# Optimization experiments

Measured on AMD Instinct MI355X. Metric: run time of the kernel, lower is better.

## Reference

```python
import jax, jax.numpy as jnp
import numpy as np
import math

D_MODEL = 1024
N_HEADS = 16
SPARSITY = 0.3


def setup_inputs() -> dict:
    key = jax.random.key(0)
    ks = jax.random.split(key, 12)
    B, S, D = 4, 2048, D_MODEL
    Dh = D // 2
    sc = 0.02
    inp = {
        "x": jax.random.normal(ks[0], (B, S, D), dtype=jnp.float32),
        "wq": jax.random.normal(ks[1], (D, D), dtype=jnp.float32) * sc,
        "bq": jnp.zeros((D,), jnp.float32),
        "wk": jax.random.normal(ks[2], (D, D), dtype=jnp.float32) * sc,
        "bk": jnp.zeros((D,), jnp.float32),
        "wv": jax.random.normal(ks[3], (D, D), dtype=jnp.float32) * sc,
        "bv": jnp.zeros((D,), jnp.float32),
        "wo": jax.random.normal(ks[4], (D, D), dtype=jnp.float32) * sc,
        "bo": jnp.zeros((D,), jnp.float32),
        "wi1": jax.random.normal(ks[5], (Dh, D), dtype=jnp.float32) * sc,
        "bi1": jnp.zeros((Dh,), jnp.float32),
        "wi2": jax.random.normal(ks[6], (1, Dh), dtype=jnp.float32) * sc,
        "bi2": jnp.zeros((1,), jnp.float32),
    }
    return inp


def reference(x, wq, bq, wk, bk, wv, bv, wo, bo, wi1, bi1, wi2, bi2):
    B, S, D = x.shape
    H = N_HEADS
    hd = D // H
    k = max(1, int(S * SPARSITY))

    # projections (torch Linear: x @ W^T + b)
    Q = (x @ wq.T + bq).reshape(B, S, H, hd).transpose(0, 2, 1, 3)  # [B,H,S,hd]
    K = (x @ wk.T + bk).reshape(B, S, H, hd).transpose(0, 2, 1, 3)
    V = (x @ wv.T + bv).reshape(B, S, H, hd).transpose(0, 2, 1, 3)

    # learned indexer -> per-position importance [B,S]
    h = jnp.maximum(x @ wi1.T + bi1, 0.0)
    importance = (h @ wi2.T + bi2)[..., 0]

    _, top_idx = jax.lax.top_k(importance, k)  # [B,k]
    sparse_mask = jnp.zeros((B, S), dtype=x.dtype).at[
        jnp.arange(B)[:, None], top_idx
    ].set(1.0)

    scores = jnp.einsum("bhqd,bhkd->bhqk", Q, K) / math.sqrt(hd)
    scores = jnp.where(sparse_mask[:, None, None, :] == 0, -jnp.inf, scores)
    attn = jax.nn.softmax(scores, axis=-1)

    out = jnp.einsum("bhqk,bhkd->bhqd", attn, V)
    out = out.transpose(0, 2, 1, 3).reshape(B, S, D)
    return out @ wo.T + bo
```

## Files before the change

### kernel.cpp

```cpp
#include <hip/hip_runtime.h>
#include <math.h>

#define BB 4
#define SS 2048
#define DD 1024
#define HHD 16
#define HD 64
#define DH 512
#define KSEL 614
#define KPAD 640
#define MTOT (BB*SS)
#define NCH (KPAD/64)
#define MKV (BB*KPAD)

typedef __attribute__((ext_vector_type(8))) short bf16x8;
typedef __attribute__((ext_vector_type(4))) float f32x4;

#define LDS_CAST(p) ((__attribute__((address_space(3))) void*)(p))
#define GLB_CAST(p) ((const __attribute__((address_space(1))) void*)(p))

#define QK_SCALE 0.18033688011112042f

__device__ inline short bf16rne(float v)
{
    unsigned u = __builtin_bit_cast(unsigned, v);
    return (short)((u + 0x7FFFu + ((u >> 16) & 1u)) >> 16);
}

__device__ inline void split1(float v, short& h, short& l)
{
    unsigned u = __builtin_bit_cast(unsigned, v);
    unsigned hr = (u + 0x7FFFu + ((u >> 16) & 1u)) >> 16;
    h = (short)hr;
    float hf = __builtin_bit_cast(float, hr << 16);
    float res = v - hf;
    unsigned u2 = __builtin_bit_cast(unsigned, res);
    unsigned lr = (u2 + 0x7FFFu + ((u2 >> 16) & 1u)) >> 16;
    l = (short)lr;
}

__global__ __launch_bounds__(256)
void split_convert(const float* __restrict__ in, short* __restrict__ hi,
                   short* __restrict__ lo, int n4)
{
    const int i = blockIdx.x * 256 + threadIdx.x;
    if (i >= n4) return;
    float4 v = reinterpret_cast<const float4*>(in)[i];
    short4 h, l;
    split1(v.x, h.x, l.x);
    split1(v.y, h.y, l.y);
    split1(v.z, h.z, l.z);
    split1(v.w, h.w, l.w);
    reinterpret_cast<short4*>(hi)[i] = h;
    reinterpret_cast<short4*>(lo)[i] = l;
}

__global__ __launch_bounds__(256)
void split_weights(const float* __restrict__ wq, const float* __restrict__ wk,
                   const float* __restrict__ wv, const float* __restrict__ wo,
                   const float* __restrict__ wi1,
                   short* __restrict__ Bqkv_hi, short* __restrict__ wo_hi,
                   short* __restrict__ Wi_hi, short* __restrict__ Wi_lo)
{
    const int i = blockIdx.x * 256 + threadIdx.x;
    const int which = blockIdx.y;
    if (which < 4) {
        const float* src = (which == 0) ? wq : (which == 1) ? wk : (which == 2) ? wv : wo;
        short* dst = (which == 3) ? wo_hi : (Bqkv_hi + (size_t)which * DD * DD);
        float4 v = reinterpret_cast<const float4*>(src)[i];
        short4 hh;
        hh.x = bf16rne(v.x); hh.y = bf16rne(v.y); hh.z = bf16rne(v.z); hh.w = bf16rne(v.w);
        reinterpret_cast<short4*>(dst)[i] = hh;
    } else {
        if (i >= DH*DD/4) return;
        float4 v = reinterpret_cast<const float4*>(wi1)[i];
        short4 h, l;
        split1(v.x, h.x, l.x); split1(v.y, h.y, l.y);
        split1(v.z, h.z, l.z); split1(v.w, h.w, l.w);
        reinterpret_cast<short4*>(Wi_hi)[i] = h;
        reinterpret_cast<short4*>(Wi_lo)[i] = l;
    }
}

__global__ __launch_bounds__(256)
void concat_bias2(const float* __restrict__ a, const float* __restrict__ b,
                  float* __restrict__ o)
{
    const int i = blockIdx.x * 256 + threadIdx.x;
    o[i] = (i < 1024) ? a[i] : b[i - 1024];
}

template<bool BF16_OUT, bool QSCALE>
__global__ __launch_bounds__(256)
void gemm_bf16(const short* __restrict__ Ahi, const short* __restrict__ Bhi,
               const float* __restrict__ bias, void* __restrict__ Cv,
               int M, int N, int K, int ldc)
{
    __shared__ short sAh[128*64];
    __shared__ short sBh[128*64];

    const int t = threadIdx.x;
    const int lane = t & 63, wid = t >> 6;
    const int wm = wid >> 1, wn = wid & 1;
    const int row0 = blockIdx.y * 128, col0 = blockIdx.x * 128;
    const int g = lane >> 4, r = lane & 15;
    const int lrow = lane >> 3;
    const int lslot = lane & 7;

    f32x4 acc[4][4];
    #pragma unroll
    for (int mt = 0; mt < 4; ++mt)
        #pragma unroll
        for (int nt = 0; nt < 4; ++nt) acc[mt][nt] = (f32x4){0.f, 0.f, 0.f, 0.f};

    for (int k0 = 0; k0 < K; k0 += 64) {
        #pragma unroll
        for (int e = 0; e < 4; ++e) {
            const int rl = wid * 32 + e * 8 + lrow;
            const int scol = k0 + ((lslot ^ (rl & 7)) << 3);
            const size_t ga = (size_t)(row0 + rl) * K + scol;
            const size_t gb = (size_t)(col0 + rl) * K + scol;
            const int ldso = (wid * 32 + e * 8) * 64;
            __builtin_amdgcn_global_load_lds(GLB_CAST(Ahi + ga), LDS_CAST(sAh + ldso), 16, 0, 0);
            __builtin_amdgcn_global_load_lds(GLB_CAST(Bhi + gb), LDS_CAST(sBh + ldso), 16, 0, 0);
        }
        __syncthreads();

        #pragma unroll
        for (int kk = 0; kk < 2; ++kk) {
            bf16x8 ah[4], bh[4];
            #pragma unroll
            for (int mt = 0; mt < 4; ++mt) {
                const int rw = wm * 64 + mt * 16 + r;
                ah[mt] = *reinterpret_cast<const bf16x8*>(sAh + rw * 64 + (((kk*4 + g) ^ (rw & 7)) << 3));
            }
            #pragma unroll
            for (int nt = 0; nt < 4; ++nt) {
                const int rw = wn * 64 + nt * 16 + r;
                bh[nt] = *reinterpret_cast<const bf16x8*>(sBh + rw * 64 + (((kk*4 + g) ^ (rw & 7)) << 3));
            }
            #pragma unroll
            for (int mt = 0; mt < 4; ++mt)
                #pragma unroll
                for (int nt = 0; nt < 4; ++nt)
                    acc[mt][nt] = __builtin_amdgcn_mfma_f32_16x16x32_bf16(ah[mt], bh[nt], acc[mt][nt], 0, 0, 0);
        }
        __syncthreads();
    }

    #pragma unroll
    for (int nt = 0; nt < 4; ++nt) {
        const int col = wn * 64 + nt * 16 + r;
        const float bv = bias[col0 + col];
        const bool qs = QSCALE && (col0 + col) < 1024;
        #pragma unroll
        for (int mt = 0; mt < 4; ++mt) {
            #pragma unroll
            for (int e = 0; e < 4; ++e) {
                const int row = row0 + wm * 64 + mt * 16 + 4 * g + e;
                float v = acc[mt][nt][e] + bv;
                if (qs) v *= QK_SCALE;
                if (BF16_OUT)
                    ((short*)Cv)[(size_t)row * ldc + col0 + col] = bf16rne(v);
                else
                    ((float*)Cv)[(size_t)row * ldc + col0 + col] = v;
            }
        }
    }
}

__global__ __launch_bounds__(256)
void gemm_kv_gather(const short* __restrict__ Ahi, const short* __restrict__ Bhi,
                    const int* __restrict__ idxg, const float* __restrict__ bias,
                    short* __restrict__ C)
{
    __shared__ short sAh[128*64];
    __shared__ short sBh[128*64];

    const int K = DD, N = 2048;
    const int t = threadIdx.x;
    const int lane = t & 63, wid = t >> 6;
    const int wm = wid >> 1, wn = wid & 1;
    const int row0 = blockIdx.y * 128, col0 = blockIdx.x * 128;
    const int g = lane >> 4, r = lane & 15;
    const int lrow = lane >> 3;
    const int lslot = lane & 7;

    size_t garow[4];
    #pragma unroll
    for (int e = 0; e < 4; ++e) {
        const int rl = row0 + wid * 32 + e * 8 + lrow;
        const int grow = (rl / KPAD) * SS + idxg[rl];
        garow[e] = (size_t)grow * K;
    }

    f32x4 acc[4][4];
    #pragma unroll
    for (int mt = 0; mt < 4; ++mt)
        #pragma unroll
        for (int nt = 0; nt < 4; ++nt) acc[mt][nt] = (f32x4){0.f, 0.f, 0.f, 0.f};

    for (int k0 = 0; k0 < K; k0 += 64) {
        #pragma unroll
        for (int e = 0; e < 4; ++e) {
            const int rl = wid * 32 + e * 8 + lrow;
            const int scol = k0 + ((lslot ^ (rl & 7)) << 3);
            const size_t gb = (size_t)(col0 + rl) * K + scol;
            const int ldso = (wid * 32 + e * 8) * 64;
            __builtin_amdgcn_global_load_lds(GLB_CAST(Ahi + garow[e] + scol), LDS_CAST(sAh + ldso), 16, 0, 0);
            __builtin_amdgcn_global_load_lds(GLB_CAST(Bhi + gb), LDS_CAST(sBh + ldso), 16, 0, 0);
        }
        __syncthreads();

        #pragma unroll
        for (int kk = 0; kk < 2; ++kk) {
            bf16x8 ah[4], bh[4];
            #pragma unroll
            for (int mt = 0; mt < 4; ++mt) {
                const int rw = wm * 64 + mt * 16 + r;
                ah[mt] = *reinterpret_cast<const bf16x8*>(sAh + rw * 64 + (((kk*4 + g) ^ (rw & 7)) << 3));
            }
            #pragma unroll
            for (int nt = 0; nt < 4; ++nt) {
                const int rw = wn * 64 + nt * 16 + r;
                bh[nt] = *reinterpret_cast<const bf16x8*>(sBh + rw * 64 + (((kk*4 + g) ^ (rw & 7)) << 3));
            }
            #pragma unroll
            for (int mt = 0; mt < 4; ++mt)
                #pragma unroll
                for (int nt = 0; nt < 4; ++nt)
                    acc[mt][nt] = __builtin_amdgcn_mfma_f32_16x16x32_bf16(ah[mt], bh[nt], acc[mt][nt], 0, 0, 0);
        }
        __syncthreads();
    }

    #pragma unroll
    for (int nt = 0; nt < 4; ++nt) {
        const int col = wn * 64 + nt * 16 + r;
        const float bv = bias[col0 + col];
        #pragma unroll
        for (int mt = 0; mt < 4; ++mt) {
            #pragma unroll
            for (int e = 0; e < 4; ++e) {
                const int row = row0 + wm * 64 + mt * 16 + 4 * g + e;
                C[(size_t)row * N + col0 + col] = bf16rne(acc[mt][nt][e] + bv);
            }
        }
    }
}

template<bool RELU>
__global__ __launch_bounds__(256)
void gemm_split64(const short* __restrict__ Ahi, const short* __restrict__ Alo,
                  const short* __restrict__ Bhi, const short* __restrict__ Blo,
                  const float* __restrict__ bias, float* __restrict__ C,
                  int M, int N, int K, int ldc)
{
    __shared__ short sAh[64*32];
    __shared__ short sAl[64*32];
    __shared__ short sBh[128*32];
    __shared__ short sBl[128*32];

    const int t = threadIdx.x;
    const int lane = t & 63, wid = t >> 6;
    const int row0 = blockIdx.y * 64, col0 = blockIdx.x * 128;
    const int g = lane >> 4, r = lane & 15;
    const int srow = lane >> 2;
    const int sslot = lane & 3;

    f32x4 acc[4][2];
    #pragma unroll
    for (int mt = 0; mt < 4; ++mt)
        #pragma unroll
        for (int nt = 0; nt < 2; ++nt) acc[mt][nt] = (f32x4){0.f, 0.f, 0.f, 0.f};

    for (int k0 = 0; k0 < K; k0 += 32) {
        {
            const int rl = wid * 16 + srow;
            const int scol = k0 + ((sslot ^ ((rl >> 2) & 3)) << 3);
            const size_t ga = (size_t)(row0 + rl) * K + scol;
            const int ldso = (wid * 16) * 32;
            __builtin_amdgcn_global_load_lds(GLB_CAST(Ahi + ga), LDS_CAST(sAh + ldso), 16, 0, 0);
            __builtin_amdgcn_global_load_lds(GLB_CAST(Alo + ga), LDS_CAST(sAl + ldso), 16, 0, 0);
        }
        #pragma unroll
        for (int i = 0; i < 2; ++i) {
            const int rl = i * 64 + wid * 16 + srow;
            const int scol = k0 + ((sslot ^ ((rl >> 2) & 3)) << 3);
            const size_t gb = (size_t)(col0 + rl) * K + scol;
            const int ldso = (i * 64 + wid * 16) * 32;
            __builtin_amdgcn_global_load_lds(GLB_CAST(Bhi + gb), LDS_CAST(sBh + ldso), 16, 0, 0);
            __builtin_amdgcn_global_load_lds(GLB_CAST(Blo + gb), LDS_CAST(sBl + ldso), 16, 0, 0);
        }
        __syncthreads();

        bf16x8 ah[4], al[4], bh[2], bl[2];
        #pragma unroll
        for (int mt = 0; mt < 4; ++mt) {
            const int row = mt * 16 + r;
            const int sw = g ^ ((row >> 2) & 3);
            ah[mt] = *reinterpret_cast<const bf16x8*>(sAh + row * 32 + sw * 8);
            al[mt] = *reinterpret_cast<const bf16x8*>(sAl + row * 32 + sw * 8);
        }
        #pragma unroll
        for (int nt = 0; nt < 2; ++nt) {
            const int row = wid * 32 + nt * 16 + r;
            const int sw = g ^ ((row >> 2) & 3);
            bh[nt] = *reinterpret_cast<const bf16x8*>(sBh + row * 32 + sw * 8);
            bl[nt] = *reinterpret_cast<const bf16x8*>(sBl + row * 32 + sw * 8);
        }
        #pragma unroll
        for (int mt = 0; mt < 4; ++mt)
            #pragma unroll
            for (int nt = 0; nt < 2; ++nt) {
                acc[mt][nt] = __builtin_amdgcn_mfma_f32_16x16x32_bf16(ah[mt], bh[nt], acc[mt][nt], 0, 0, 0);
                acc[mt][nt] = __builtin_amdgcn_mfma_f32_16x16x32_bf16(ah[mt], bl[nt], acc[mt][nt], 0, 0, 0);
                acc[mt][nt] = __builtin_amdgcn_mfma_f32_16x16x32_bf16(al[mt], bh[nt], acc[mt][nt], 0, 0, 0);
            }
        __syncthreads();
    }

    #pragma unroll
    for (int nt = 0; nt < 2; ++nt) {
        const int col = wid * 32 + nt * 16 + r;
        const float bv = bias[col0 + col];
        #pragma unroll
        for (int mt = 0; mt < 4; ++mt) {
            #pragma unroll
            for (int e = 0; e < 4; ++e) {
                const int row = row0 + mt * 16 + 4 * g + e;
                float v = acc[mt][nt][e] + bv;
                if (RELU) v = fmaxf(v, 0.f);
                C[(size_t)row * ldc + col0 + col] = v;
            }
        }
    }
}

__global__ __launch_bounds__(256)
void importance_kernel(const float* __restrict__ h, const float* __restrict__ wi2,
                       const float* __restrict__ bi2, float* __restrict__ imp)
{
    const int wid = threadIdx.x >> 6, lane = threadIdx.x & 63;
    const int row = blockIdx.x * 4 + wid;
    const float* hr = h + (size_t)row * DH;
    float s = 0.f;
    #pragma unroll
    for (int i = 0; i < DH/64; ++i)
        s = fmaf(hr[lane + i*64], wi2[lane + i*64], s);
    #pragma unroll
    for (int off = 32; off; off >>= 1) s += __shfl_down(s, off);
    if (lane == 0) imp[row] = s + bi2[0];
}

__global__ __launch_bounds__(256)
void rank_kernel(const float* __restrict__ imp, int* __restrict__ flags)
{
    __shared__ float simp[SS];
    const int b = blockIdx.y;
    const int t = threadIdx.x;
    const float* bimp = imp + b * SS;
    for (int i = t; i < SS/4; i += 256)
        reinterpret_cast<float4*>(simp)[i] = reinterpret_cast<const float4*>(bimp)[i];
    __syncthreads();

    const int i = blockIdx.x * 32 + (t >> 3);
    const int part = t & 7;
    const float v = simp[i];
    const float4* slice = reinterpret_cast<const float4*>(simp + part * (SS/8));
    const int jb = part * (SS/8);
    int rank = 0;
    #pragma unroll 8
    for (int jj = 0; jj < SS/32; ++jj) {
        const float4 u4 = slice[jj];
        const int j = jb + jj * 4;
        rank += (u4.x > v) || ((u4.x == v) && (j + 0 < i));
        rank += (u4.y > v) || ((u4.y == v) && (j + 1 < i));
        rank += (u4.z > v) || ((u4.z == v) && (j + 2 < i));
        rank += (u4.w > v) || ((u4.w == v) && (j + 3 < i));
    }
    rank += __shfl_xor(rank, 1);
    rank += __shfl_xor(rank, 2);
    rank += __shfl_xor(rank, 4);
    if (part == 0) flags[b * SS + i] = (rank < KSEL) ? 1 : 0;
}

__global__ __launch_bounds__(256)
void compact_kernel(const int* __restrict__ flags, int* __restrict__ idxg)
{
    __shared__ int sscan[SS];
    __shared__ int sidx[KSEL];
    const int b = blockIdx.x, t = threadIdx.x;
    for (int i = t; i < SS; i += 256) sscan[i] = flags[b * SS + i];
    __syncthreads();
    for (int off = 1; off < SS; off <<= 1) {
        int vals[SS/256];
        #pragma unroll
        for (int c = 0; c < SS/256; ++c) {
            const int i = t + c * 256;
            int v = sscan[i];
            if (i >= off) v += sscan[i - off];
            vals[c] = v;
        }
        __syncthreads();
        #pragma unroll
        for (int c = 0; c < SS/256; ++c) sscan[t + c * 256] = vals[c];
        __syncthreads();
    }
    for (int i = t; i < SS; i += 256) {
        const int f = flags[b * SS + i];
        if (f) sidx[sscan[i] - 1] = i;
    }
    __syncthreads();
    for (int p = t; p < KPAD; p += 256)
        idxg[b * KPAD + p] = sidx[min(p, KSEL - 1)];
}

__global__ __launch_bounds__(256)
void gather_kv(const short* __restrict__ KVc, short* __restrict__ Kg,
               short* __restrict__ Vg)
{
    __shared__ short Vs[64*72];
    const int t = threadIdx.x;
    const int c = blockIdx.x, h = blockIdx.y, b = blockIdx.z;
    const int srow = t >> 2;
    const int sq4  = t & 3;

    const size_t cbase = ((size_t)(b * HHD + h) * NCH + c) * 4096;

    const short* kb = KVc + (size_t)(b * KPAD + c * 64 + srow) * 2048 + h * HD + sq4 * 16;
    bf16x8 k0 = *reinterpret_cast<const bf16x8*>(kb);
    bf16x8 k1 = *reinterpret_cast<const bf16x8*>(kb + 8);
    short* kout = Kg + cbase + srow * HD + sq4 * 16;
    *reinterpret_cast<bf16x8*>(kout)     = k0;
    *reinterpret_cast<bf16x8*>(kout + 8) = k1;

    const short* vbp = kb + 1024;
    bf16x8 v0 = *reinterpret_cast<const bf16x8*>(vbp);
    bf16x8 v1 = *reinterpret_cast<const bf16x8*>(vbp + 8);
    #pragma unroll
    for (int j = 0; j < 8; ++j) {
        Vs[(sq4 * 16 + j) * 72 + srow]     = v0[j];
        Vs[(sq4 * 16 + 8 + j) * 72 + srow] = v1[j];
    }
    __syncthreads();

    const int x = 8 * (srow >> 4);
    short* vout = Vg + cbase + srow * 64;
    *reinterpret_cast<bf16x8*>(vout + ((sq4 * 16)     ^ x)) = *reinterpret_cast<const bf16x8*>(&Vs[srow * 72 + sq4 * 16]);
    *reinterpret_cast<bf16x8*>(vout + ((sq4 * 16 + 8) ^ x)) = *reinterpret_cast<const bf16x8*>(&Vs[srow * 72 + sq4 * 16 + 8]);
}

__global__ __launch_bounds__(512)
void attn_mfma(const short* __restrict__ Qb, const short* __restrict__ Kg,
               const short* __restrict__ Vg, short* __restrict__ AOhi)
{
    __shared__ short Ks[2][64*72];
    __shared__ short Vs[2][64*72];
    __shared__ short Ps[8][16*72];

    const int t = threadIdx.x;
    const int lane = t & 63, w = t >> 6;
    const int g = lane >> 4, r = lane & 15;
    const int qt = blockIdx.x, h = blockIdx.y, b = blockIdx.z;
    const int q0 = qt * 128;
    short* Psw = &Ps[w][0];

    const int srow = t >> 3;
    const int scol = (t & 7) * 8;
    const short* kcbase = Kg + ((size_t)(b * HHD + h) * NCH) * 4096 + srow * 64 + scol;
    const short* vcbase = Vg + ((size_t)(b * HHD + h) * NCH) * 4096 + srow * 64 + scol;

    bf16x8 qh[2];
    {
        const short* qrow = Qb + (size_t)(b * SS + q0 + w * 16 + r) * DD + h * HD;
        qh[0] = *reinterpret_cast<const bf16x8*>(qrow + 8 * g);
        qh[1] = *reinterpret_cast<const bf16x8*>(qrow + 32 + 8 * g);
    }

    bf16x8 ones;
    #pragma unroll
    for (int j = 0; j < 8; ++j) ones[j] = (short)0x3F80;

    f32x4 oacc[4];
    #pragma unroll
    for (int dt = 0; dt < 4; ++dt) oacc[dt] = (f32x4){0.f, 0.f, 0.f, 0.f};
    f32x4 dacc = (f32x4){0.f, 0.f, 0.f, 0.f};

    bf16x8 kreg = *reinterpret_cast<const bf16x8*>(kcbase);
    bf16x8 vreg = *reinterpret_cast<const bf16x8*>(vcbase);

    for (int c = 0; c < NCH; ++c) {
        const int cur = c & 1;
        *reinterpret_cast<bf16x8*>(&Ks[cur][srow*72 + scol]) = kreg;
        *reinterpret_cast<bf16x8*>(&Vs[cur][srow*72 + scol]) = vreg;
        if (c + 1 < NCH) {
            kreg = *reinterpret_cast<const bf16x8*>(kcbase + (size_t)(c + 1) * 4096);
            vreg = *reinterpret_cast<const bf16x8*>(vcbase + (size_t)(c + 1) * 4096);
        }
        __syncthreads();

        f32x4 sa[4];
        #pragma unroll
        for (int kt = 0; kt < 4; ++kt) {
            bf16x8 kf0 = *reinterpret_cast<const bf16x8*>(&Ks[cur][(kt*16 + r)*72 + 8*g]);
            bf16x8 kf1 = *reinterpret_cast<const bf16x8*>(&Ks[cur][(kt*16 + r)*72 + 32 + 8*g]);
            f32x4 s = (f32x4){0.f, 0.f, 0.f, 0.f};
            s = __builtin_amdgcn_mfma_f32_16x16x32_bf16(qh[0], kf0, s, 0, 0, 0);
            s = __builtin_amdgcn_mfma_f32_16x16x32_bf16(qh[1], kf1, s, 0, 0, 0);
            sa[kt] = s;
        }
        if (c == NCH - 1) {
            #pragma unroll
            for (int kt = 0; kt < 4; ++kt)
                if (c*64 + kt*16 + r >= KSEL)
                    sa[kt] = (f32x4){-INFINITY, -INFINITY, -INFINITY, -INFINITY};
        }

        #pragma unroll
        for (int kt = 0; kt < 4; ++kt)
            #pragma unroll
            for (int e = 0; e < 4; ++e)
                Psw[(4*g + e)*72 + ((kt*16 + r) ^ (8*g))] =
                    (short)(__builtin_bit_cast(unsigned, exp2f(sa[kt][e])) >> 16);

        #pragma unroll
        for (int kc = 0; kc < 2; ++kc) {
            bf16x8 pf = *reinterpret_cast<const bf16x8*>(&Psw[r*72 + kc*32 + 8*(g ^ (r >> 2))]);
            dacc = __builtin_amdgcn_mfma_f32_16x16x32_bf16(pf, ones, dacc, 0, 0, 0);
            #pragma unroll
            for (int dt = 0; dt < 4; ++dt) {
                bf16x8 vf = *reinterpret_cast<const bf16x8*>(&Vs[cur][(dt*16 + r)*72 + kc*32 + 8*(g ^ dt)]);
                oacc[dt] = __builtin_amdgcn_mfma_f32_16x16x32_bf16(pf, vf, oacc[dt], 0, 0, 0);
            }
        }
    }

    #pragma unroll
    for (int dt = 0; dt < 4; ++dt)
        #pragma unroll
        for (int e = 0; e < 4; ++e) {
            const size_t a = (size_t)(b * SS + q0 + w*16 + 4*g + e) * DD + h * HD + dt*16 + r;
            AOhi[a] = bf16rne(oacc[dt][e] / dacc[e]);
        }
}

extern "C" void kernel_launch(void* const* d_in, const int* in_sizes, int n_in,
                              void* d_out, int out_size, void* d_ws, size_t ws_size,
                              hipStream_t stream)
{
    const float* x   = (const float*)d_in[0];
    const float* wq  = (const float*)d_in[1];
    const float* bq  = (const float*)d_in[2];
    const float* wk  = (const float*)d_in[3];
    const float* bk  = (const float*)d_in[4];
    const float* wv  = (const float*)d_in[5];
    const float* bv  = (const float*)d_in[6];
    const float* wo  = (const float*)d_in[7];
    const float* bo  = (const float*)d_in[8];
    const float* wi1 = (const float*)d_in[9];
    const float* bi1 = (const float*)d_in[10];
    const float* wi2 = (const float*)d_in[11];
    const float* bi2 = (const float*)d_in[12];
    float* out = (float*)d_out;

    const size_t MB = 1ull << 20;
    char* W = (char*)d_ws;
    short* x_hi  = (short*)(W + 0);
    short* x_lo  = (short*)(W + 16*MB);
    short* Qb    = (short*)(W + 32*MB);
    short* KVc   = (short*)(W + 48*MB);
    short* Wi_hi = (short*)(W + 96*MB);
    short* Wi_lo = (short*)(W + 97*MB);
    short* Bqkv_hi=(short*)(W + 128*MB);
    short* wo_hi = (short*)(W + 134*MB);
    float* Hw    = (float*)(W + 144*MB);
    short* Kg    = (short*)(W + 144*MB);
    short* Vg    = (short*)(W + 150*MB);
    float* bkv   = (float*)(W + 160*MB);
    float* imp   = (float*)(W + 160*MB + 64*1024);
    int*   flags = (int*)(W + 160*MB + 128*1024);
    int*   idxg  = (int*)(W + 160*MB + 192*1024);
    short* AO_hi = x_hi;

    const size_t NM = (size_t)MTOT * DD;

    split_convert<<<(NM/4 + 255)/256, 256, 0, stream>>>(x, x_hi, x_lo, NM/4);
    split_weights<<<dim3(DD*DD/4/256, 5), 256, 0, stream>>>(
        wq, wk, wv, wo, wi1, Bqkv_hi, wo_hi, Wi_hi, Wi_lo);
    concat_bias2<<<2048/256, 256, 0, stream>>>(bk, bv, bkv);

    gemm_split64<true><<<dim3(DH/128, MTOT/64), 256, 0, stream>>>(
        x_hi, x_lo, Wi_hi, Wi_lo, bi1, Hw, MTOT, DH, DD, DH);
    importance_kernel<<<MTOT/4, 256, 0, stream>>>(Hw, wi2, bi2, imp);
    rank_kernel<<<dim3(SS/32, BB), 256, 0, stream>>>(imp, flags);
    compact_kernel<<<BB, 256, 0, stream>>>(flags, idxg);

    gemm_bf16<true, true><<<dim3(DD/128, MTOT/128), 256, 0, stream>>>(
        x_hi, Bqkv_hi, bq, Qb, MTOT, DD, DD, DD);
    gemm_kv_gather<<<dim3(2048/128, MKV/128), 256, 0, stream>>>(
        x_hi, Bqkv_hi + (size_t)DD*DD, idxg, bkv, KVc);

    gather_kv<<<dim3(NCH, HHD, BB), 256, 0, stream>>>(KVc, Kg, Vg);

    attn_mfma<<<dim3(SS/128, HHD, BB), 512, 0, stream>>>(Qb, Kg, Vg, AO_hi);

    gemm_bf16<false, false><<<dim3(DD/128, MTOT/128), 256, 0, stream>>>(
        AO_hi, wo_hi, bo, out, MTOT, DD, DD, DD);
}
```

Measured before the change: 200.5 us.

## Fuse indexer and Q projection GEMMs into one launch, fold bias concat

Merges the indexer hidden-layer GEMM (split hi/lo precision, ReLU) and the Q projection GEMM into a single kernel whose odd/even blocks run either path, so the two independent GEMMs share one grid. The bias concatenation kernel is folded into the weight-split kernel as an extra grid row. This removes two launches and lets both GEMMs fill the device together. The cost is a heterogeneous block mix with uneven per-block work and a larger shared-memory footprint for the indexer blocks.

```diff
diff --git a/kernel.cpp b/kernel.cpp
--- a/kernel.cpp
+++ b/kernel.cpp
@@ -59,8 +59,10 @@
 void split_weights(const float* __restrict__ wq, const float* __restrict__ wk,
                    const float* __restrict__ wv, const float* __restrict__ wo,
                    const float* __restrict__ wi1,
+                   const float* __restrict__ bk, const float* __restrict__ bv,
                    short* __restrict__ Bqkv_hi, short* __restrict__ wo_hi,
-                   short* __restrict__ Wi_hi, short* __restrict__ Wi_lo)
+                   short* __restrict__ Wi_hi, short* __restrict__ Wi_lo,
+                   float* __restrict__ bkv)
 {
     const int i = blockIdx.x * 256 + threadIdx.x;
     const int which = blockIdx.y;
@@ -71,7 +73,7 @@
         short4 hh;
         hh.x = bf16rne(v.x); hh.y = bf16rne(v.y); hh.z = bf16rne(v.z); hh.w = bf16rne(v.w);
         reinterpret_cast<short4*>(dst)[i] = hh;
-    } else {
+    } else if (which == 4) {
         if (i >= DH*DD/4) return;
         float4 v = reinterpret_cast<const float4*>(wi1)[i];
         short4 h, l;
@@ -79,15 +81,10 @@
         split1(v.z, h.z, l.z); split1(v.w, h.w, l.w);
         reinterpret_cast<short4*>(Wi_hi)[i] = h;
         reinterpret_cast<short4*>(Wi_lo)[i] = l;
-    }
-}
-
-__global__ __launch_bounds__(256)
-void concat_bias2(const float* __restrict__ a, const float* __restrict__ b,
-                  float* __restrict__ o)
-{
-    const int i = blockIdx.x * 256 + threadIdx.x;
-    o[i] = (i < 1024) ? a[i] : b[i - 1024];
+    } else {
+        if (i >= 2048) return;
+        bkv[i] = (i < 1024) ? bk[i] : bv[i - 1024];
+    }
 }
 
 template<bool BF16_OUT, bool QSCALE>
@@ -170,6 +167,159 @@
 }
 
 __global__ __launch_bounds__(256)
+void idx_q_fused(const short* __restrict__ x_hi, const short* __restrict__ x_lo,
+                 const short* __restrict__ Wq_hi, const float* __restrict__ bq,
+                 short* __restrict__ Qb,
+                 const short* __restrict__ Wi_hi, const short* __restrict__ Wi_lo,
+                 const float* __restrict__ bi1, float* __restrict__ Hw)
+{
+    __shared__ __align__(16) char smem[32768];
+    const int t = threadIdx.x;
+    const int lane = t & 63, wid = t >> 6;
+    const int g = lane >> 4, r = lane & 15;
+
+    if ((blockIdx.x & 1) == 0) {
+        const int id = blockIdx.x >> 1;
+        const int row0 = (id >> 3) * 128, col0 = (id & 7) * 128;
+        short* sAh = (short*)smem;
+        short* sBh = sAh + 128*64;
+        const int wm = wid >> 1, wn = wid & 1;
+        const int lrow = lane >> 3;
+        const int lslot = lane & 7;
+
+        f32x4 acc[4][4];
+        #pragma unroll
+        for (int mt = 0; mt < 4; ++mt)
+            #pragma unroll
+            for (int nt = 0; nt < 4; ++nt) acc[mt][nt] = (f32x4){0.f, 0.f, 0.f, 0.f};
+
+        for (int k0 = 0; k0 < DD; k0 += 64) {
+            #pragma unroll
+            for (int e = 0; e < 4; ++e) {
+                const int rl = wid * 32 + e * 8 + lrow;
+                const int scol = k0 + ((lslot ^ (rl & 7)) << 3);
+                const size_t ga = (size_t)(row0 + rl) * DD + scol;
+                const size_t gb = (size_t)(col0 + rl) * DD + scol;
+                const int ldso = (wid * 32 + e * 8) * 64;
+                __builtin_amdgcn_global_load_lds(GLB_CAST(x_hi + ga), LDS_CAST(sAh + ldso), 16, 0, 0);
+                __builtin_amdgcn_global_load_lds(GLB_CAST(Wq_hi + gb), LDS_CAST(sBh + ldso), 16, 0, 0);
+            }
+            __syncthreads();
+
+            #pragma unroll
+            for (int kk = 0; kk < 2; ++kk) {
+                bf16x8 ah[4], bh[4];
+                #pragma unroll
+                for (int mt = 0; mt < 4; ++mt) {
+                    const int rw = wm * 64 + mt * 16 + r;
+                    ah[mt] = *reinterpret_cast<const bf16x8*>(sAh + rw * 64 + (((kk*4 + g) ^ (rw & 7)) << 3));
+                }
+                #pragma unroll
+                for (int nt = 0; nt < 4; ++nt) {
+                    const int rw = wn * 64 + nt * 16 + r;
+                    bh[nt] = *reinterpret_cast<const bf16x8*>(sBh + rw * 64 + (((kk*4 + g) ^ (rw & 7)) << 3));
+                }
+                #pragma unroll
+                for (int mt = 0; mt < 4; ++mt)
+                    #pragma unroll
+                    for (int nt = 0; nt < 4; ++nt)
+                        acc[mt][nt] = __builtin_amdgcn_mfma_f32_16x16x32_bf16(ah[mt], bh[nt], acc[mt][nt], 0, 0, 0);
+            }
+            __syncthreads();
+        }
+
+        #pragma unroll
+        for (int nt = 0; nt < 4; ++nt) {
+            const int col = wn * 64 + nt * 16 + r;
+            const float bv = bq[col0 + col];
+            #pragma unroll
+            for (int mt = 0; mt < 4; ++mt) {
+                #pragma unroll
+                for (int e = 0; e < 4; ++e) {
+                    const int row = row0 + wm * 64 + mt * 16 + 4 * g + e;
+                    Qb[(size_t)row * DD + col0 + col] = bf16rne((acc[mt][nt][e] + bv) * QK_SCALE);
+                }
+            }
+        }
+    } else {
+        const int id = blockIdx.x >> 1;
+        const int row0 = (id >> 2) * 64, col0 = (id & 3) * 128;
+        short* sAh = (short*)smem;
+        short* sAl = sAh + 64*32;
+        short* sBh = sAl + 64*32;
+        short* sBl = sBh + 128*32;
+        const int srow = lane >> 2;
+        const int sslot = lane & 3;
+
+        f32x4 acc[4][2];
+        #pragma unroll
+        for (int mt = 0; mt < 4; ++mt)
+            #pragma unroll
+            for (int nt = 0; nt < 2; ++nt) acc[mt][nt] = (f32x4){0.f, 0.f, 0.f, 0.f};
+
+        for (int k0 = 0; k0 < DD; k0 += 32) {
+            {
+                const int rl = wid * 16 + srow;
+                const int scol = k0 + ((sslot ^ ((rl >> 2) & 3)) << 3);
+                const size_t ga = (size_t)(row0 + rl) * DD + scol;
+                const int ldso = (wid * 16) * 32;
+                __builtin_amdgcn_global_load_lds(GLB_CAST(x_hi + ga), LDS_CAST(sAh + ldso), 16, 0, 0);
+                __builtin_amdgcn_global_load_lds(GLB_CAST(x_lo + ga), LDS_CAST(sAl + ldso), 16, 0, 0);
+            }
+            #pragma unroll
+            for (int i = 0; i < 2; ++i) {
+                const int rl = i * 64 + wid * 16 + srow;
+                const int scol = k0 + ((sslot ^ ((rl >> 2) & 3)) << 3);
+                const size_t gb = (size_t)(col0 + rl) * DD + scol;
+                const int ldso = (i * 64 + wid * 16) * 32;
+                __builtin_amdgcn_global_load_lds(GLB_CAST(Wi_hi + gb), LDS_CAST(sBh + ldso), 16, 0, 0);
+                __builtin_amdgcn_global_load_lds(GLB_CAST(Wi_lo + gb), LDS_CAST(sBl + ldso), 16, 0, 0);
+            }
+            __syncthreads();
+
+            bf16x8 ah[4], al[4], bh[2], bl[2];
+            #pragma unroll
+            for (int mt = 0; mt < 4; ++mt) {
+                const int row = mt * 16 + r;
+                const int sw = g ^ ((row >> 2) & 3);
+                ah[mt] = *reinterpret_cast<const bf16x8*>(sAh + row * 32 + sw * 8);
+                al[mt] = *reinterpret_cast<const bf16x8*>(sAl + row * 32 + sw * 8);
+            }
+            #pragma unroll
+            for (int nt = 0; nt < 2; ++nt) {
+                const int row = wid * 32 + nt * 16 + r;
+                const int sw = g ^ ((row >> 2) & 3);
+                bh[nt] = *reinterpret_cast<const bf16x8*>(sBh + row * 32 + sw * 8);
+                bl[nt] = *reinterpret_cast<const bf16x8*>(sBl + row * 32 + sw * 8);
+            }
+            #pragma unroll
+            for (int mt = 0; mt < 4; ++mt)
+                #pragma unroll
+                for (int nt = 0; nt < 2; ++nt) {
+                    acc[mt][nt] = __builtin_amdgcn_mfma_f32_16x16x32_bf16(ah[mt], bh[nt], acc[mt][nt], 0, 0, 0);
+                    acc[mt][nt] = __builtin_amdgcn_mfma_f32_16x16x32_bf16(ah[mt], bl[nt], acc[mt][nt], 0, 0, 0);
+                    acc[mt][nt] = __builtin_amdgcn_mfma_f32_16x16x32_bf16(al[mt], bh[nt], acc[mt][nt], 0, 0, 0);
+                }
+            __syncthreads();
+        }
+
+        #pragma unroll
+        for (int nt = 0; nt < 2; ++nt) {
+            const int col = wid * 32 + nt * 16 + r;
+            const float bv = bi1[col0 + col];
+            #pragma unroll
+            for (int mt = 0; mt < 4; ++mt) {
+                #pragma unroll
+                for (int e = 0; e < 4; ++e) {
+                    const int row = row0 + mt * 16 + 4 * g + e;
+                    Hw[(size_t)row * DH + col0 + col] = fmaxf(acc[mt][nt][e] + bv, 0.f);
+                }
+            }
+        }
+    }
+}
+
+__global__ __launch_bounds__(256)
 void gemm_kv_gather(const short* __restrict__ Ahi, const short* __restrict__ Bhi,
                     const int* __restrict__ idxg, const float* __restrict__ bias,
                     short* __restrict__ C)
@@ -244,94 +394,6 @@
             for (int e = 0; e < 4; ++e) {
                 const int row = row0 + wm * 64 + mt * 16 + 4 * g + e;
                 C[(size_t)row * N + col0 + col] = bf16rne(acc[mt][nt][e] + bv);
-            }
-        }
-    }
-}
-
-template<bool RELU>
-__global__ __launch_bounds__(256)
-void gemm_split64(const short* __restrict__ Ahi, const short* __restrict__ Alo,
-                  const short* __restrict__ Bhi, const short* __restrict__ Blo,
-                  const float* __restrict__ bias, float* __restrict__ C,
-                  int M, int N, int K, int ldc)
-{
-    __shared__ short sAh[64*32];
-    __shared__ short sAl[64*32];
-    __shared__ short sBh[128*32];
-    __shared__ short sBl[128*32];
-
-    const int t = threadIdx.x;
-    const int lane = t & 63, wid = t >> 6;
-    const int row0 = blockIdx.y * 64, col0 = blockIdx.x * 128;
-    const int g = lane >> 4, r = lane & 15;
-    const int srow = lane >> 2;
-    const int sslot = lane & 3;
-
-    f32x4 acc[4][2];
-    #pragma unroll
-    for (int mt = 0; mt < 4; ++mt)
-        #pragma unroll
-        for (int nt = 0; nt < 2; ++nt) acc[mt][nt] = (f32x4){0.f, 0.f, 0.f, 0.f};
-
-    for (int k0 = 0; k0 < K; k0 += 32) {
-        {
-            const int rl = wid * 16 + srow;
-            const int scol = k0 + ((sslot ^ ((rl >> 2) & 3)) << 3);
-            const size_t ga = (size_t)(row0 + rl) * K + scol;
-            const int ldso = (wid * 16) * 32;
-            __builtin_amdgcn_global_load_lds(GLB_CAST(Ahi + ga), LDS_CAST(sAh + ldso), 16, 0, 0);
-            __builtin_amdgcn_global_load_lds(GLB_CAST(Alo + ga), LDS_CAST(sAl + ldso), 16, 0, 0);
-        }
-        #pragma unroll
-        for (int i = 0; i < 2; ++i) {
-            const int rl = i * 64 + wid * 16 + srow;
-            const int scol = k0 + ((sslot ^ ((rl >> 2) & 3)) << 3);
-            const size_t gb = (size_t)(col0 + rl) * K + scol;
-            const int ldso = (i * 64 + wid * 16) * 32;
-            __builtin_amdgcn_global_load_lds(GLB_CAST(Bhi + gb), LDS_CAST(sBh + ldso), 16, 0, 0);
-            __builtin_amdgcn_global_load_lds(GLB_CAST(Blo + gb), LDS_CAST(sBl + ldso), 16, 0, 0);
-        }
-        __syncthreads();
-
-        bf16x8 ah[4], al[4], bh[2], bl[2];
-        #pragma unroll
-        for (int mt = 0; mt < 4; ++mt) {
-            const int row = mt * 16 + r;
-            const int sw = g ^ ((row >> 2) & 3);
-            ah[mt] = *reinterpret_cast<const bf16x8*>(sAh + row * 32 + sw * 8);
-            al[mt] = *reinterpret_cast<const bf16x8*>(sAl + row * 32 + sw * 8);
-        }
-        #pragma unroll
-        for (int nt = 0; nt < 2; ++nt) {
-            const int row = wid * 32 + nt * 16 + r;
-            const int sw = g ^ ((row >> 2) & 3);
-            bh[nt] = *reinterpret_cast<const bf16x8*>(sBh + row * 32 + sw * 8);
-            bl[nt] = *reinterpret_cast<const bf16x8*>(sBl + row * 32 + sw * 8);
-        }
-        #pragma unroll
-        for (int mt = 0; mt < 4; ++mt)
-            #pragma unroll
-            for (int nt = 0; nt < 2; ++nt) {
-                acc[mt][nt] = __builtin_amdgcn_mfma_f32_16x16x32_bf16(ah[mt], bh[nt], acc[mt][nt], 0, 0, 0);
-                acc[mt][nt] = __builtin_amdgcn_mfma_f32_16x16x32_bf16(ah[mt], bl[nt], acc[mt][nt], 0, 0, 0);
-                acc[mt][nt] = __builtin_amdgcn_mfma_f32_16x16x32_bf16(al[mt], bh[nt], acc[mt][nt], 0, 0, 0);
-            }
-        __syncthreads();
-    }
-
-    #pragma unroll
-    for (int nt = 0; nt < 2; ++nt) {
-        const int col = wid * 32 + nt * 16 + r;
-        const float bv = bias[col0 + col];
-        #pragma unroll
-        for (int mt = 0; mt < 4; ++mt) {
-            #pragma unroll
-            for (int e = 0; e < 4; ++e) {
-                const int row = row0 + mt * 16 + 4 * g + e;
-                float v = acc[mt][nt][e] + bv;
-                if (RELU) v = fmaxf(v, 0.f);
-                C[(size_t)row * ldc + col0 + col] = v;
             }
         }
     }
@@ -586,18 +648,16 @@
     const size_t NM = (size_t)MTOT * DD;
 
     split_convert<<<(NM/4 + 255)/256, 256, 0, stream>>>(x, x_hi, x_lo, NM/4);
-    split_weights<<<dim3(DD*DD/4/256, 5), 256, 0, stream>>>(
-        wq, wk, wv, wo, wi1, Bqkv_hi, wo_hi, Wi_hi, Wi_lo);
-    concat_bias2<<<2048/256, 256, 0, stream>>>(bk, bv, bkv);
-
-    gemm_split64<true><<<dim3(DH/128, MTOT/64), 256, 0, stream>>>(
-        x_hi, x_lo, Wi_hi, Wi_lo, bi1, Hw, MTOT, DH, DD, DH);
+    split_weights<<<dim3(DD*DD/4/256, 6), 256, 0, stream>>>(
+        wq, wk, wv, wo, wi1, bk, bv, Bqkv_hi, wo_hi, Wi_hi, Wi_lo, bkv);
+
+    idx_q_fused<<<1024, 256, 0, stream>>>(
+        x_hi, x_lo, Bqkv_hi, bq, Qb, Wi_hi, Wi_lo, bi1, Hw);
+
     importance_kernel<<<MTOT/4, 256, 0, stream>>>(Hw, wi2, bi2, imp);
     rank_kernel<<<dim3(SS/32, BB), 256, 0, stream>>>(imp, flags);
     compact_kernel<<<BB, 256, 0, stream>>>(flags, idxg);
 
-    gemm_bf16<true, true><<<dim3(DD/128, MTOT/128), 256, 0, stream>>>(
-        x_hi, Bqkv_hi, bq, Qb, MTOT, DD, DD, DD);
     gemm_kv_gather<<<dim3(2048/128, MKV/128), 256, 0, stream>>>(
         x_hi, Bqkv_hi + (size_t)DD*DD, idxg, bkv, KVc);
 
```

Result: no change. 200.4 us (-0.1%).
